# Performance work log

Measured on AMD Instinct MI355X. Metric: run time of the kernel, lower is better.

The kernel has to match this reference:

```python
import jax, jax.numpy as jnp
import numpy as np
import math

EPS = 1e-6
TEMPERATURE = 1.0
NEG = -100.0


def setup_inputs() -> dict:
    key = jax.random.key(0)
    k1, k2, k3 = jax.random.split(key, 3)
    B, N, C = 16, 2048, 64
    x = jax.random.normal(k1, (B, N, C), dtype=jnp.float32)
    y = jax.random.normal(k2, (B, N, C), dtype=jnp.float32)
    # complementary keep / pruned gates, as produced by the TPS token scorer
    keep = jax.random.bernoulli(k3, 0.5, (B, N, 1)).astype(jnp.float32)
    pruned = 1.0 - keep
    return {
        "x": x,
        "y": y,
        "current_keep_decision": keep,
        "current_pruned_decision": pruned,
    }


def reference(x, y, current_keep_decision, current_pruned_decision):
    # Training branch of TPSModule.forward (module defaults to training mode).
    B, N, C = x.shape
    # --- get_sim(x, None, mask_eye=-100, l2_norm=True) ---
    xn = x / (jnp.linalg.norm(x, axis=-1, keepdims=True) + EPS)
    sim = jnp.einsum("bnc,bmc->bnm", xn, xn)  # [B, N, N]
    eye = jnp.eye(N, dtype=bool)
    sim = jnp.where(eye[None, :, :], NEG, sim)
    sim = sim / TEMPERATURE
    # mask out columns of non-kept tokens
    keep_b = current_keep_decision.reshape(B, 1, N).astype(bool)
    sim = jnp.where(keep_b, sim, NEG)
    # hard top-1 (with ties) per row, gated by pruned flag of the source row
    sim_th = jnp.max(sim, axis=2, keepdims=True)  # [B, N, 1]
    mask = (sim == sim_th).astype(x.dtype) * current_pruned_decision  # [B, N, N]
    cos = mask * sim
    # transpose: now rows index destination (kept) tokens
    mask_t = mask.transpose(0, 2, 1)
    cos_t = cos.transpose(0, 2, 1)
    numerator = jnp.exp(cos_t) * mask_t  # [B, N, N]
    denominator = math.e + jnp.sum(numerator, axis=-1, keepdims=True)  # [B, N, 1]
    out = x * (math.e / denominator) + jnp.einsum(
        "bnm,bmc->bnc", numerator / denominator, x
    )
    return out
```

## Files before the change

### kernel.cpp

```cpp
#include <hip/hip_runtime.h>
#include <math.h>

#define BB 16
#define NN 2048
#define CC 64
#define TPB 256
#define MAXT 72
#define IVN (MAXT * 16)
#define E_CONST 2.71828182845904523536f

typedef __attribute__((ext_vector_type(8))) short bf16x8;
typedef __attribute__((ext_vector_type(4))) float f32x4;
#define MFMA(A_, B_, C_) __builtin_amdgcn_mfma_f32_16x16x32_bf16(A_, B_, C_, 0, 0, 0)

__device__ __forceinline__ unsigned short rnbf16(float v) {
    unsigned u = __float_as_uint(v);
    return (unsigned short)((u + 0x7FFFu + ((u >> 16) & 1u)) >> 16);
}
__device__ __forceinline__ float bf2f(unsigned short h) {
    return __uint_as_float((unsigned)h << 16);
}

__global__ __launch_bounds__(TPB) void k_pre(const float* __restrict__ keep,
                                             float* __restrict__ outz,
                                             float* __restrict__ S,
                                             int* __restrict__ cntP,
                                             int* __restrict__ cntK,
                                             int* __restrict__ listP,
                                             int* __restrict__ listK) {
    const int tid = threadIdx.x, lane = tid & 63;

    float4* o4 = (float4*)outz + (size_t)blockIdx.x * 1024;
    float4 z = {0.0f, 0.0f, 0.0f, 0.0f};
#pragma unroll
    for (int i = 0; i < 4; ++i) o4[i * TPB + tid] = z;

    const int b = blockIdx.x;
    if (b >= BB) return;

    __shared__ int cP, cK;
    if (tid == 0) { cP = 0; cK = 0; }
    __syncthreads();
    for (int i = tid; i < NN; i += TPB) S[b * NN + i] = 0.0f;
    const unsigned long long lt = (lane == 63) ? 0x7fffffffffffffffull
                                               : ((1ull << lane) - 1ull);
#pragma unroll
    for (int it = 0; it < NN / TPB; ++it) {
        int n = it * TPB + tid;
        bool kp = keep[b * NN + n] != 0.0f;
        unsigned long long mk = __ballot(kp);
        int nk = __popcll(mk);
        int bk = 0, bp = 0;
        if (lane == 0) {
            bk = atomicAdd(&cK, nk);
            bp = atomicAdd(&cP, 64 - nk);
        }
        bk = __shfl(bk, 0); bp = __shfl(bp, 0);
        int pk = __popcll(mk & lt);
        if (kp) listK[b * NN + bk + pk] = n;
        else    listP[b * NN + bp + (lane - pk)] = n;
    }
    __syncthreads();
    if (tid == 0) { cntP[b] = cP; cntK[b] = cK; }
}

__global__ __launch_bounds__(TPB) void k_pack(const float* __restrict__ x,
                                              const int* __restrict__ cnt,
                                              const int* __restrict__ list,
                                              float4* __restrict__ outF,
                                              float* __restrict__ ivrOut,
                                              int normalize) {
    const int b = blockIdx.x & 15;
    const int t = blockIdx.x >> 4;
    const int lane = threadIdx.x & 63;
    const int wid  = threadIdx.x >> 6;
    const int C = cnt[b];
    __shared__ float4 stage4[384];
    unsigned short* st = (unsigned short*)stage4;
    const float* xb = x + (size_t)b * NN * CC;

    const int g  = (lane >> 3) & 3;
    const int kf = lane >> 5;
    const int e  = lane & 7;
#pragma unroll
    for (int it = 0; it < 4; ++it) {
        int ci = wid * 4 + it;
        int cp = t * 16 + ci;
        float v = 0.0f;
        if (cp < C) {
            int tok = list[b * NN + cp];
            float xv = xb[(size_t)tok * CC + lane];
            float sq = xv * xv;
#pragma unroll
            for (int off = 32; off; off >>= 1) sq += __shfl_xor(sq, off, 64);
            float ivr = 1.0f / (sqrtf(sq) + 1e-6f);
            if (ivrOut && lane == 0) ivrOut[b * IVN + cp] = ivr;
            v = normalize ? xv * ivr : xv;
        }
        unsigned short hb = rnbf16(v);
        float r1 = v - bf2f(hb);
        unsigned short mb = rnbf16(r1);
        float r2 = r1 - bf2f(mb);
        unsigned short lb = rnbf16(r2);
        int lt = ci + g * 16;
        st[((0 + kf) * 64 + lt) * 8 + e] = hb;
        st[((2 + kf) * 64 + lt) * 8 + e] = mb;
        st[((4 + kf) * 64 + lt) * 8 + e] = lb;
    }
    __syncthreads();
    float4* dst = outF + (size_t)(b * MAXT + t) * 384;
    for (int i = threadIdx.x; i < 384; i += TPB) dst[i] = stage4[i];
}

__global__ __launch_bounds__(TPB) void k_argmax(
    const float* __restrict__ x,
    const float4* __restrict__ colA,
    const float4* __restrict__ rowB,
    const float* __restrict__ ivrArr,
    const int* __restrict__ cntP, const int* __restrict__ cntK,
    const int* __restrict__ listP, const int* __restrict__ listK,
    float* __restrict__ S,
    float* __restrict__ A) {

    const int b  = blockIdx.x & 15;
    const int rt = blockIdx.x >> 4;
    const int P = cntP[b], K = cntK[b];
    const int base = rt * 16;
    if (base >= P) return;

    const int lane = threadIdx.x & 63;
    const int wid  = threadIdx.x >> 6;

    const float4* rb = rowB + (size_t)(b * MAXT + rt) * 384;
    bf16x8 B0h = __builtin_bit_cast(bf16x8, rb[0 * 64 + lane]);
    bf16x8 B1h = __builtin_bit_cast(bf16x8, rb[1 * 64 + lane]);
    bf16x8 B0m = __builtin_bit_cast(bf16x8, rb[2 * 64 + lane]);
    bf16x8 B1m = __builtin_bit_cast(bf16x8, rb[3 * 64 + lane]);
    bf16x8 B0l = __builtin_bit_cast(bf16x8, rb[4 * 64 + lane]);
    bf16x8 B1l = __builtin_bit_cast(bf16x8, rb[5 * 64 + lane]);

    float tmax = -3.0e38f;
    unsigned long long mskA = 0ull, mskB = 0ull;
    const int NT = (K + 15) >> 4;
    const float4* ca = colA + (size_t)b * MAXT * 384;
    const int cgrp = (lane >> 4) << 2;

    int i = 0;
    for (int t = wid; t < NT; t += 4, ++i) {
        const float4* af = ca + (size_t)t * 384;
        bf16x8 A0h = __builtin_bit_cast(bf16x8, af[0 * 64 + lane]);
        bf16x8 A1h = __builtin_bit_cast(bf16x8, af[1 * 64 + lane]);
        bf16x8 A0m = __builtin_bit_cast(bf16x8, af[2 * 64 + lane]);
        bf16x8 A1m = __builtin_bit_cast(bf16x8, af[3 * 64 + lane]);
        bf16x8 A0l = __builtin_bit_cast(bf16x8, af[4 * 64 + lane]);
        bf16x8 A1l = __builtin_bit_cast(bf16x8, af[5 * 64 + lane]);

        f32x4 accS = {0.f, 0.f, 0.f, 0.f}, accH = {0.f, 0.f, 0.f, 0.f};
        accS = MFMA(A0m, B0m, accS); accS = MFMA(A1m, B1m, accS);
        accS = MFMA(A0h, B0l, accS); accS = MFMA(A1h, B1l, accS);
        accS = MFMA(A0l, B0h, accS); accS = MFMA(A1l, B1h, accS);
        accH = MFMA(A0h, B0m, accH); accH = MFMA(A1h, B1m, accH);
        accH = MFMA(A0m, B0h, accH); accH = MFMA(A1m, B1h, accH);
        accH = MFMA(A0h, B0h, accH); accH = MFMA(A1h, B1h, accH);

        const int cb = t * 16 + cgrp;
        const int ib = (i & 15) << 2;
#pragma unroll
        for (int j = 0; j < 4; ++j) {
            float s = accH[j] + accS[j];
            s = (cb + j < K) ? s : -3.0e38f;
            unsigned long long bit = 1ull << (ib | j);
            if (i < 16) {
                if (s > tmax)       { tmax = s; mskA = bit; mskB = 0ull; }
                else if (s == tmax) mskA |= bit;
            } else {
                if (s > tmax)       { tmax = s; mskB = bit; mskA = 0ull; }
                else if (s == tmax) mskB |= bit;
            }
        }
    }

    float m = tmax;
    m = fmaxf(m, __shfl_xor(m, 16, 64));
    m = fmaxf(m, __shfl_xor(m, 32, 64));
    __shared__ float mW[16][4];
    if (lane < 16) mW[lane][wid] = m;
    __syncthreads();

    const int nvr = min(16, P - base);
    for (int r = 0; r < nvr; ++r) {
        float M = fmaxf(fmaxf(mW[r][0], mW[r][1]), fmaxf(mW[r][2], mW[r][3]));
        unsigned long long bal = __ballot((lane & 15) == r && tmax == M);
        if (bal == 0ull) continue;
        int src = listP[b * NN + base + r];
        float ivr = ivrArr[b * IVN + base + r];
        float wgt = expf(M * ivr);
        float xv = x[((size_t)b * NN + src) * CC + lane];
        while (bal) {
            int sl = __ffsll(bal) - 1;
            bal &= bal - 1;
            unsigned long long mA = __shfl(mskA, sl);
            unsigned long long mB = __shfl(mskB, sl);
            int cg = (sl >> 4) << 2;
            while (mA) {
                int bb = __ffsll(mA) - 1; mA &= mA - 1;
                int colp = (wid + 4 * (bb >> 2)) * 16 + cg + (bb & 3);
                int dst = listK[b * NN + colp];
                atomicAdd(&A[((size_t)b * NN + dst) * CC + lane], wgt * xv);
                if (lane == 0) atomicAdd(&S[b * NN + dst], wgt);
            }
            while (mB) {
                int bb = __ffsll(mB) - 1; mB &= mB - 1;
                int colp = (wid + 4 * (16 + (bb >> 2))) * 16 + cg + (bb & 3);
                int dst = listK[b * NN + colp];
                atomicAdd(&A[((size_t)b * NN + dst) * CC + lane], wgt * xv);
                if (lane == 0) atomicAdd(&S[b * NN + dst], wgt);
            }
        }
    }
}

__global__ __launch_bounds__(TPB) void k_finalize(const float* __restrict__ x,
                                                  const float* __restrict__ S,
                                                  float* __restrict__ out) {
    int i = blockIdx.x * TPB + threadIdx.x;
    int row = i >> 4;
    float inv = 1.0f / (E_CONST + S[row]);
    float4 xv = ((const float4*)x)[i];
    float4 av = ((float4*)out)[i];
    float4 o;
    o.x = (xv.x * E_CONST + av.x) * inv;
    o.y = (xv.y * E_CONST + av.y) * inv;
    o.z = (xv.z * E_CONST + av.z) * inv;
    o.w = (xv.w * E_CONST + av.w) * inv;
    ((float4*)out)[i] = o;
}

extern "C" void kernel_launch(void* const* d_in, const int* in_sizes, int n_in,
                              void* d_out, int out_size, void* d_ws, size_t ws_size,
                              hipStream_t stream) {
    const float* x    = (const float*)d_in[0];
    const float* keep = (const float*)d_in[2];
    float* out = (float*)d_out;

    char* ws = (char*)d_ws;
    float* S     = (float*)(ws + (128 << 10));
    int*   cntP  = (int*)(ws + (256 << 10));
    int*   cntK  = cntP + 16;
    int*   listP = (int*)(ws + (256 << 10) + 128);
    int*   listK = listP + BB * NN;
    float* ivrArr = (float*)(ws + (768 << 10));
    float4* colA = (float4*)(ws + (1 << 20));
    float4* rowB = (float4*)(ws + (8 << 20));

    k_pre<<<512, TPB, 0, stream>>>(keep, out, S, cntP, cntK, listP, listK);

    k_pack<<<BB * MAXT, TPB, 0, stream>>>(x, cntK, listK, colA, nullptr, 1);
    k_pack<<<BB * MAXT, TPB, 0, stream>>>(x, cntP, listP, rowB, ivrArr, 0);

    k_argmax<<<2048, TPB, 0, stream>>>(x, colA, rowB, ivrArr,
                                       cntP, cntK, listP, listK, S, out);

    k_finalize<<<(BB * NN * CC / 4) / TPB, TPB, 0, stream>>>(x, S, out);
}
```

Baseline: 120.6 us.

## Process two row tiles per argmax block and merge pack launches

The argmax kernel now handles 32 pruned rows per block instead of 16. Each loaded column tile (A fragments) is reused across two row tiles, which halves the column-fragment global loads and gives each wave twice as many independent MFMA chains. The two k_pack launches are merged into one grid, with blockIdx selecting the keep or pruned list, to save a kernel launch. The cost is roughly double the register use for B fragments and masks, and half as many argmax blocks, which lowers parallelism.

```diff
diff --git a/kernel.cpp b/kernel.cpp
--- a/kernel.cpp
+++ b/kernel.cpp
@@ -65,16 +65,24 @@
 }
 
 __global__ __launch_bounds__(TPB) void k_pack(const float* __restrict__ x,
-                                              const int* __restrict__ cnt,
-                                              const int* __restrict__ list,
-                                              float4* __restrict__ outF,
-                                              float* __restrict__ ivrOut,
-                                              int normalize) {
-    const int b = blockIdx.x & 15;
-    const int t = blockIdx.x >> 4;
+                                              const int* __restrict__ cntK,
+                                              const int* __restrict__ listK,
+                                              float4* __restrict__ colA,
+                                              const int* __restrict__ cntP,
+                                              const int* __restrict__ listP,
+                                              float4* __restrict__ rowB,
+                                              float* __restrict__ ivrArr) {
+    int id = blockIdx.x;
+    const bool isA = id < BB * MAXT;
+    if (!isA) id -= BB * MAXT;
+    const int b = id & 15;
+    const int t = id >> 4;
+    const int C = isA ? cntK[b] : cntP[b];
+    const int* __restrict__ list = isA ? listK : listP;
+    float4* __restrict__ outF = isA ? colA : rowB;
+
     const int lane = threadIdx.x & 63;
     const int wid  = threadIdx.x >> 6;
-    const int C = cnt[b];
     __shared__ float4 stage4[384];
     unsigned short* st = (unsigned short*)stage4;
     const float* xb = x + (size_t)b * NN * CC;
@@ -94,8 +102,8 @@
 #pragma unroll
             for (int off = 32; off; off >>= 1) sq += __shfl_xor(sq, off, 64);
             float ivr = 1.0f / (sqrtf(sq) + 1e-6f);
-            if (ivrOut && lane == 0) ivrOut[b * IVN + cp] = ivr;
-            v = normalize ? xv * ivr : xv;
+            if (!isA && lane == 0) ivrArr[b * IVN + cp] = ivr;
+            v = isA ? xv * ivr : xv;
         }
         unsigned short hb = rnbf16(v);
         float r1 = v - bf2f(hb);
@@ -125,22 +133,29 @@
     const int b  = blockIdx.x & 15;
     const int rt = blockIdx.x >> 4;
     const int P = cntP[b], K = cntK[b];
-    const int base = rt * 16;
+    const int base = rt * 32;
     if (base >= P) return;
 
     const int lane = threadIdx.x & 63;
     const int wid  = threadIdx.x >> 6;
 
-    const float4* rb = rowB + (size_t)(b * MAXT + rt) * 384;
-    bf16x8 B0h = __builtin_bit_cast(bf16x8, rb[0 * 64 + lane]);
-    bf16x8 B1h = __builtin_bit_cast(bf16x8, rb[1 * 64 + lane]);
-    bf16x8 B0m = __builtin_bit_cast(bf16x8, rb[2 * 64 + lane]);
-    bf16x8 B1m = __builtin_bit_cast(bf16x8, rb[3 * 64 + lane]);
-    bf16x8 B0l = __builtin_bit_cast(bf16x8, rb[4 * 64 + lane]);
-    bf16x8 B1l = __builtin_bit_cast(bf16x8, rb[5 * 64 + lane]);
-
-    float tmax = -3.0e38f;
-    unsigned long long mskA = 0ull, mskB = 0ull;
+    const float4* rb0 = rowB + (size_t)(b * MAXT + 2 * rt) * 384;
+    const float4* rb1 = rb0 + 384;
+    bf16x8 B0h0 = __builtin_bit_cast(bf16x8, rb0[0 * 64 + lane]);
+    bf16x8 B1h0 = __builtin_bit_cast(bf16x8, rb0[1 * 64 + lane]);
+    bf16x8 B0m0 = __builtin_bit_cast(bf16x8, rb0[2 * 64 + lane]);
+    bf16x8 B1m0 = __builtin_bit_cast(bf16x8, rb0[3 * 64 + lane]);
+    bf16x8 B0l0 = __builtin_bit_cast(bf16x8, rb0[4 * 64 + lane]);
+    bf16x8 B1l0 = __builtin_bit_cast(bf16x8, rb0[5 * 64 + lane]);
+    bf16x8 B0h1 = __builtin_bit_cast(bf16x8, rb1[0 * 64 + lane]);
+    bf16x8 B1h1 = __builtin_bit_cast(bf16x8, rb1[1 * 64 + lane]);
+    bf16x8 B0m1 = __builtin_bit_cast(bf16x8, rb1[2 * 64 + lane]);
+    bf16x8 B1m1 = __builtin_bit_cast(bf16x8, rb1[3 * 64 + lane]);
+    bf16x8 B0l1 = __builtin_bit_cast(bf16x8, rb1[4 * 64 + lane]);
+    bf16x8 B1l1 = __builtin_bit_cast(bf16x8, rb1[5 * 64 + lane]);
+
+    float tmax0 = -3.0e38f, tmax1 = -3.0e38f;
+    unsigned long long mA0 = 0ull, mB0 = 0ull, mA1 = 0ull, mB1 = 0ull;
     const int NT = (K + 15) >> 4;
     const float4* ca = colA + (size_t)b * MAXT * 384;
     const int cgrp = (lane >> 4) << 2;
@@ -155,42 +170,58 @@
         bf16x8 A0l = __builtin_bit_cast(bf16x8, af[4 * 64 + lane]);
         bf16x8 A1l = __builtin_bit_cast(bf16x8, af[5 * 64 + lane]);
 
-        f32x4 accS = {0.f, 0.f, 0.f, 0.f}, accH = {0.f, 0.f, 0.f, 0.f};
-        accS = MFMA(A0m, B0m, accS); accS = MFMA(A1m, B1m, accS);
-        accS = MFMA(A0h, B0l, accS); accS = MFMA(A1h, B1l, accS);
-        accS = MFMA(A0l, B0h, accS); accS = MFMA(A1l, B1h, accS);
-        accH = MFMA(A0h, B0m, accH); accH = MFMA(A1h, B1m, accH);
-        accH = MFMA(A0m, B0h, accH); accH = MFMA(A1m, B1h, accH);
-        accH = MFMA(A0h, B0h, accH); accH = MFMA(A1h, B1h, accH);
+        f32x4 accS0 = {0.f,0.f,0.f,0.f}, accH0 = {0.f,0.f,0.f,0.f};
+        f32x4 accS1 = {0.f,0.f,0.f,0.f}, accH1 = {0.f,0.f,0.f,0.f};
+        accS0 = MFMA(A0m, B0m0, accS0); accS0 = MFMA(A1m, B1m0, accS0);
+        accS1 = MFMA(A0m, B0m1, accS1); accS1 = MFMA(A1m, B1m1, accS1);
+        accS0 = MFMA(A0h, B0l0, accS0); accS0 = MFMA(A1h, B1l0, accS0);
+        accS1 = MFMA(A0h, B0l1, accS1); accS1 = MFMA(A1h, B1l1, accS1);
+        accS0 = MFMA(A0l, B0h0, accS0); accS0 = MFMA(A1l, B1h0, accS0);
+        accS1 = MFMA(A0l, B0h1, accS1); accS1 = MFMA(A1l, B1h1, accS1);
+        accH0 = MFMA(A0h, B0m0, accH0); accH0 = MFMA(A1h, B1m0, accH0);
+        accH1 = MFMA(A0h, B0m1, accH1); accH1 = MFMA(A1h, B1m1, accH1);
+        accH0 = MFMA(A0m, B0h0, accH0); accH0 = MFMA(A1m, B1h0, accH0);
+        accH1 = MFMA(A0m, B0h1, accH1); accH1 = MFMA(A1m, B1h1, accH1);
+        accH0 = MFMA(A0h, B0h0, accH0); accH0 = MFMA(A1h, B1h0, accH0);
+        accH1 = MFMA(A0h, B0h1, accH1); accH1 = MFMA(A1h, B1h1, accH1);
 
         const int cb = t * 16 + cgrp;
         const int ib = (i & 15) << 2;
 #pragma unroll
         for (int j = 0; j < 4; ++j) {
-            float s = accH[j] + accS[j];
-            s = (cb + j < K) ? s : -3.0e38f;
+            float s0 = accH0[j] + accS0[j];
+            float s1 = accH1[j] + accS1[j];
+            bool ok = (cb + j < K);
+            s0 = ok ? s0 : -3.0e38f;
+            s1 = ok ? s1 : -3.0e38f;
             unsigned long long bit = 1ull << (ib | j);
             if (i < 16) {
-                if (s > tmax)       { tmax = s; mskA = bit; mskB = 0ull; }
-                else if (s == tmax) mskA |= bit;
+                if (s0 > tmax0)       { tmax0 = s0; mA0 = bit; mB0 = 0ull; }
+                else if (s0 == tmax0)  mA0 |= bit;
+                if (s1 > tmax1)       { tmax1 = s1; mA1 = bit; mB1 = 0ull; }
+                else if (s1 == tmax1)  mA1 |= bit;
             } else {
-                if (s > tmax)       { tmax = s; mskB = bit; mskA = 0ull; }
-                else if (s == tmax) mskB |= bit;
+                if (s0 > tmax0)       { tmax0 = s0; mB0 = bit; mA0 = 0ull; }
+                else if (s0 == tmax0)  mB0 |= bit;
+                if (s1 > tmax1)       { tmax1 = s1; mB1 = bit; mA1 = 0ull; }
+                else if (s1 == tmax1)  mB1 |= bit;
             }
         }
     }
 
-    float m = tmax;
-    m = fmaxf(m, __shfl_xor(m, 16, 64));
-    m = fmaxf(m, __shfl_xor(m, 32, 64));
-    __shared__ float mW[16][4];
-    if (lane < 16) mW[lane][wid] = m;
-    __syncthreads();
-
-    const int nvr = min(16, P - base);
+    float m0 = tmax0, m1 = tmax1;
+    m0 = fmaxf(m0, __shfl_xor(m0, 16, 64)); m0 = fmaxf(m0, __shfl_xor(m0, 32, 64));
+    m1 = fmaxf(m1, __shfl_xor(m1, 16, 64)); m1 = fmaxf(m1, __shfl_xor(m1, 32, 64));
+    __shared__ float mW[32][4];
+    if (lane < 16) { mW[lane][wid] = m0; mW[16 + lane][wid] = m1; }
+    __syncthreads();
+
+    const int nvr = min(32, P - base);
     for (int r = 0; r < nvr; ++r) {
+        const int half = r >> 4;
         float M = fmaxf(fmaxf(mW[r][0], mW[r][1]), fmaxf(mW[r][2], mW[r][3]));
-        unsigned long long bal = __ballot((lane & 15) == r && tmax == M);
+        float myT = half ? tmax1 : tmax0;
+        unsigned long long bal = __ballot((lane & 15) == (r & 15) && myT == M);
         if (bal == 0ull) continue;
         int src = listP[b * NN + base + r];
         float ivr = ivrArr[b * IVN + base + r];
@@ -199,18 +230,18 @@
         while (bal) {
             int sl = __ffsll(bal) - 1;
             bal &= bal - 1;
-            unsigned long long mA = __shfl(mskA, sl);
-            unsigned long long mB = __shfl(mskB, sl);
+            unsigned long long mAs = __shfl(half ? mA1 : mA0, sl);
+            unsigned long long mBs = __shfl(half ? mB1 : mB0, sl);
             int cg = (sl >> 4) << 2;
-            while (mA) {
-                int bb = __ffsll(mA) - 1; mA &= mA - 1;
+            while (mAs) {
+                int bb = __ffsll(mAs) - 1; mAs &= mAs - 1;
                 int colp = (wid + 4 * (bb >> 2)) * 16 + cg + (bb & 3);
                 int dst = listK[b * NN + colp];
                 atomicAdd(&A[((size_t)b * NN + dst) * CC + lane], wgt * xv);
                 if (lane == 0) atomicAdd(&S[b * NN + dst], wgt);
             }
-            while (mB) {
-                int bb = __ffsll(mB) - 1; mB &= mB - 1;
+            while (mBs) {
+                int bb = __ffsll(mBs) - 1; mBs &= mBs - 1;
                 int colp = (wid + 4 * (16 + (bb >> 2))) * 16 + cg + (bb & 3);
                 int dst = listK[b * NN + colp];
                 atomicAdd(&A[((size_t)b * NN + dst) * CC + lane], wgt * xv);
@@ -255,10 +286,10 @@
 
     k_pre<<<512, TPB, 0, stream>>>(keep, out, S, cntP, cntK, listP, listK);
 
-    k_pack<<<BB * MAXT, TPB, 0, stream>>>(x, cntK, listK, colA, nullptr, 1);
-    k_pack<<<BB * MAXT, TPB, 0, stream>>>(x, cntP, listP, rowB, ivrArr, 0);
-
-    k_argmax<<<2048, TPB, 0, stream>>>(x, colA, rowB, ivrArr,
+    k_pack<<<2 * BB * MAXT, TPB, 0, stream>>>(x, cntK, listK, colA,
+                                              cntP, listP, rowB, ivrArr);
+
+    k_argmax<<<1024, TPB, 0, stream>>>(x, colA, rowB, ivrArr,
                                        cntP, cntK, listP, listK, S, out);
 
     k_finalize<<<(BB * NN * CC / 4) / TPB, TPB, 0, stream>>>(x, S, out);
```

Result: slower. 123.5 us (+2.4%).

## Merge pack launches and double-buffer A tile loads in argmax loop

Applied to the files above, without the earlier changes.

Both k_pack launches (kept-column normalized and pruned-row raw) become one grid of twice the size, with a block-index branch choosing which list and output to use. This drops one kernel launch and lets the two packing passes run concurrently. The argmax inner loop now ping-pongs between two register sets, prefetching the next column tile's six bf16 fragments while MFMAs run on the current tile, to hide global load latency. The extra fragment registers raise VGPR pressure and may lower occupancy.

```diff
diff --git a/kernel.cpp b/kernel.cpp
--- a/kernel.cpp
+++ b/kernel.cpp
@@ -65,16 +65,24 @@
 }
 
 __global__ __launch_bounds__(TPB) void k_pack(const float* __restrict__ x,
-                                              const int* __restrict__ cnt,
-                                              const int* __restrict__ list,
-                                              float4* __restrict__ outF,
-                                              float* __restrict__ ivrOut,
-                                              int normalize) {
-    const int b = blockIdx.x & 15;
-    const int t = blockIdx.x >> 4;
+                                              const int* __restrict__ cntK,
+                                              const int* __restrict__ listK,
+                                              float4* __restrict__ colA,
+                                              const int* __restrict__ cntP,
+                                              const int* __restrict__ listP,
+                                              float4* __restrict__ rowB,
+                                              float* __restrict__ ivrArr) {
+    int id = blockIdx.x;
+    const bool isA = id < BB * MAXT;
+    if (!isA) id -= BB * MAXT;
+    const int b = id & 15;
+    const int t = id >> 4;
+    const int C = isA ? cntK[b] : cntP[b];
+    const int* __restrict__ list = isA ? listK : listP;
+    float4* __restrict__ outF = isA ? colA : rowB;
+
     const int lane = threadIdx.x & 63;
     const int wid  = threadIdx.x >> 6;
-    const int C = cnt[b];
     __shared__ float4 stage4[384];
     unsigned short* st = (unsigned short*)stage4;
     const float* xb = x + (size_t)b * NN * CC;
@@ -94,8 +102,8 @@
 #pragma unroll
             for (int off = 32; off; off >>= 1) sq += __shfl_xor(sq, off, 64);
             float ivr = 1.0f / (sqrtf(sq) + 1e-6f);
-            if (ivrOut && lane == 0) ivrOut[b * IVN + cp] = ivr;
-            v = normalize ? xv * ivr : xv;
+            if (!isA && lane == 0) ivrArr[b * IVN + cp] = ivr;
+            v = isA ? xv * ivr : xv;
         }
         unsigned short hb = rnbf16(v);
         float r1 = v - bf2f(hb);
@@ -112,6 +120,47 @@
     for (int i = threadIdx.x; i < 384; i += TPB) dst[i] = stage4[i];
 }
 
+__device__ __forceinline__ void loadA6(const float4* __restrict__ af, int lane,
+                                       bf16x8& h0, bf16x8& h1, bf16x8& m0,
+                                       bf16x8& m1, bf16x8& l0, bf16x8& l1) {
+    h0 = __builtin_bit_cast(bf16x8, af[0 * 64 + lane]);
+    h1 = __builtin_bit_cast(bf16x8, af[1 * 64 + lane]);
+    m0 = __builtin_bit_cast(bf16x8, af[2 * 64 + lane]);
+    m1 = __builtin_bit_cast(bf16x8, af[3 * 64 + lane]);
+    l0 = __builtin_bit_cast(bf16x8, af[4 * 64 + lane]);
+    l1 = __builtin_bit_cast(bf16x8, af[5 * 64 + lane]);
+}
+
+__device__ __forceinline__ void computeTile(
+    bf16x8 A0h, bf16x8 A1h, bf16x8 A0m, bf16x8 A1m, bf16x8 A0l, bf16x8 A1l,
+    bf16x8 B0h, bf16x8 B1h, bf16x8 B0m, bf16x8 B1m, bf16x8 B0l, bf16x8 B1l,
+    int t, int i, int K, int cgrp,
+    float& tmax, unsigned long long& mskA, unsigned long long& mskB) {
+    f32x4 accS = {0.f, 0.f, 0.f, 0.f}, accH = {0.f, 0.f, 0.f, 0.f};
+    accS = MFMA(A0m, B0m, accS); accS = MFMA(A1m, B1m, accS);
+    accS = MFMA(A0h, B0l, accS); accS = MFMA(A1h, B1l, accS);
+    accS = MFMA(A0l, B0h, accS); accS = MFMA(A1l, B1h, accS);
+    accH = MFMA(A0h, B0m, accH); accH = MFMA(A1h, B1m, accH);
+    accH = MFMA(A0m, B0h, accH); accH = MFMA(A1m, B1h, accH);
+    accH = MFMA(A0h, B0h, accH); accH = MFMA(A1h, B1h, accH);
+
+    const int cb = t * 16 + cgrp;
+    const int ib = (i & 15) << 2;
+#pragma unroll
+    for (int j = 0; j < 4; ++j) {
+        float s = accH[j] + accS[j];
+        s = (cb + j < K) ? s : -3.0e38f;
+        unsigned long long bit = 1ull << (ib | j);
+        if (i < 16) {
+            if (s > tmax)       { tmax = s; mskA = bit; mskB = 0ull; }
+            else if (s == tmax)  mskA |= bit;
+        } else {
+            if (s > tmax)       { tmax = s; mskB = bit; mskA = 0ull; }
+            else if (s == tmax)  mskB |= bit;
+        }
+    }
+}
+
 __global__ __launch_bounds__(TPB) void k_argmax(
     const float* __restrict__ x,
     const float4* __restrict__ colA,
@@ -132,12 +181,8 @@
     const int wid  = threadIdx.x >> 6;
 
     const float4* rb = rowB + (size_t)(b * MAXT + rt) * 384;
-    bf16x8 B0h = __builtin_bit_cast(bf16x8, rb[0 * 64 + lane]);
-    bf16x8 B1h = __builtin_bit_cast(bf16x8, rb[1 * 64 + lane]);
-    bf16x8 B0m = __builtin_bit_cast(bf16x8, rb[2 * 64 + lane]);
-    bf16x8 B1m = __builtin_bit_cast(bf16x8, rb[3 * 64 + lane]);
-    bf16x8 B0l = __builtin_bit_cast(bf16x8, rb[4 * 64 + lane]);
-    bf16x8 B1l = __builtin_bit_cast(bf16x8, rb[5 * 64 + lane]);
+    bf16x8 B0h, B1h, B0m, B1m, B0l, B1l;
+    loadA6(rb, lane, B0h, B1h, B0m, B1m, B0l, B1l);
 
     float tmax = -3.0e38f;
     unsigned long long mskA = 0ull, mskB = 0ull;
@@ -145,39 +190,29 @@
     const float4* ca = colA + (size_t)b * MAXT * 384;
     const int cgrp = (lane >> 4) << 2;
 
-    int i = 0;
-    for (int t = wid; t < NT; t += 4, ++i) {
-        const float4* af = ca + (size_t)t * 384;
-        bf16x8 A0h = __builtin_bit_cast(bf16x8, af[0 * 64 + lane]);
-        bf16x8 A1h = __builtin_bit_cast(bf16x8, af[1 * 64 + lane]);
-        bf16x8 A0m = __builtin_bit_cast(bf16x8, af[2 * 64 + lane]);
-        bf16x8 A1m = __builtin_bit_cast(bf16x8, af[3 * 64 + lane]);
-        bf16x8 A0l = __builtin_bit_cast(bf16x8, af[4 * 64 + lane]);
-        bf16x8 A1l = __builtin_bit_cast(bf16x8, af[5 * 64 + lane]);
-
-        f32x4 accS = {0.f, 0.f, 0.f, 0.f}, accH = {0.f, 0.f, 0.f, 0.f};
-        accS = MFMA(A0m, B0m, accS); accS = MFMA(A1m, B1m, accS);
-        accS = MFMA(A0h, B0l, accS); accS = MFMA(A1h, B1l, accS);
-        accS = MFMA(A0l, B0h, accS); accS = MFMA(A1l, B1h, accS);
-        accH = MFMA(A0h, B0m, accH); accH = MFMA(A1h, B1m, accH);
-        accH = MFMA(A0m, B0h, accH); accH = MFMA(A1m, B1h, accH);
-        accH = MFMA(A0h, B0h, accH); accH = MFMA(A1h, B1h, accH);
-
-        const int cb = t * 16 + cgrp;
-        const int ib = (i & 15) << 2;
-#pragma unroll
-        for (int j = 0; j < 4; ++j) {
-            float s = accH[j] + accS[j];
-            s = (cb + j < K) ? s : -3.0e38f;
-            unsigned long long bit = 1ull << (ib | j);
-            if (i < 16) {
-                if (s > tmax)       { tmax = s; mskA = bit; mskB = 0ull; }
-                else if (s == tmax) mskA |= bit;
-            } else {
-                if (s > tmax)       { tmax = s; mskB = bit; mskA = 0ull; }
-                else if (s == tmax) mskB |= bit;
-            }
-        }
+    const int ntw = (NT - wid + 3) >> 2;
+    bf16x8 Aa0h, Aa1h, Aa0m, Aa1m, Aa0l, Aa1l;
+    bf16x8 Ab0h, Ab1h, Ab0m, Ab1m, Ab0l, Ab1l;
+
+    if (ntw > 0)
+        loadA6(ca + (size_t)wid * 384, lane, Aa0h, Aa1h, Aa0m, Aa1m, Aa0l, Aa1l);
+    int k = 0;
+    while (k < ntw) {
+        if (k + 1 < ntw)
+            loadA6(ca + (size_t)(wid + 4 * (k + 1)) * 384, lane,
+                   Ab0h, Ab1h, Ab0m, Ab1m, Ab0l, Ab1l);
+        computeTile(Aa0h, Aa1h, Aa0m, Aa1m, Aa0l, Aa1l,
+                    B0h, B1h, B0m, B1m, B0l, B1l,
+                    wid + 4 * k, k, K, cgrp, tmax, mskA, mskB);
+        ++k;
+        if (k >= ntw) break;
+        if (k + 1 < ntw)
+            loadA6(ca + (size_t)(wid + 4 * (k + 1)) * 384, lane,
+                   Aa0h, Aa1h, Aa0m, Aa1m, Aa0l, Aa1l);
+        computeTile(Ab0h, Ab1h, Ab0m, Ab1m, Ab0l, Ab1l,
+                    B0h, B1h, B0m, B1m, B0l, B1l,
+                    wid + 4 * k, k, K, cgrp, tmax, mskA, mskB);
+        ++k;
     }
 
     float m = tmax;
@@ -255,8 +290,8 @@
 
     k_pre<<<512, TPB, 0, stream>>>(keep, out, S, cntP, cntK, listP, listK);
 
-    k_pack<<<BB * MAXT, TPB, 0, stream>>>(x, cntK, listK, colA, nullptr, 1);
-    k_pack<<<BB * MAXT, TPB, 0, stream>>>(x, cntP, listP, rowB, ivrArr, 0);
+    k_pack<<<2 * BB * MAXT, TPB, 0, stream>>>(x, cntK, listK, colA,
+                                              cntP, listP, rowB, ivrArr);
 
     k_argmax<<<2048, TPB, 0, stream>>>(x, colA, rowB, ivrArr,
                                        cntP, cntK, listP, listK, S, out);
```

New measurement: 122.8 us. No clear change (+1.9%).
